# Kernel tuning notes

Measured on AMD Instinct MI355X. Metric: run time of the kernel, lower is better.

Reference implementation:

```python
import jax, jax.numpy as jnp
import numpy as np

N_CONS = 100_000
N_VAR = 200_000
N_EDGE = 2_000_000
EMB = 64
CONS_F = 5
VAR_F = 19
EDGE_F = 1
N_LAYERS = 2


def setup_inputs() -> dict:
    key = jax.random.key(0)
    ks = iter(jax.random.split(key, 48))
    def nrm(shape, scale=0.05):
        return jax.random.normal(next(ks), shape, dtype=jnp.float32) * scale
    inp = {}
    inp["cons_x"] = jax.random.normal(next(ks), (N_CONS, CONS_F), dtype=jnp.float32)
    inp["var_x"] = jax.random.normal(next(ks), (N_VAR, VAR_F), dtype=jnp.float32)
    row = jax.random.randint(next(ks), (N_EDGE,), 0, N_CONS, dtype=jnp.int32)
    col = jax.random.randint(next(ks), (N_EDGE,), 0, N_VAR, dtype=jnp.int32)
    inp["edge_index"] = jnp.stack([row, col], axis=0)
    inp["edge_attr"] = jax.random.normal(next(ks), (N_EDGE, EDGE_F), dtype=jnp.float32)
    inp["break_indicator"] = jax.random.uniform(next(ks), (N_VAR, 1), dtype=jnp.float32)
    # PreNormLayer affine params: y = (x + shift) * scale
    inp["cons_pn_shift"] = nrm((CONS_F,))
    inp["cons_pn_scale"] = 1.0 + nrm((CONS_F,))
    inp["var_pn_shift"] = nrm((VAR_F,))
    inp["var_pn_scale"] = 1.0 + nrm((VAR_F,))
    inp["edge_pn_shift"] = nrm((EDGE_F,))
    inp["edge_pn_scale"] = 1.0 + nrm((EDGE_F,))
    # embedding MLPs
    inp["cons_W1"] = nrm((CONS_F, EMB), 0.4)
    inp["cons_b1"] = nrm((EMB,))
    inp["cons_W2"] = nrm((EMB, EMB), 0.12)
    inp["cons_b2"] = nrm((EMB,))
    inp["var_W1"] = nrm((VAR_F, EMB), 0.22)
    inp["var_b1"] = nrm((EMB,))
    inp["var_W2"] = nrm((EMB, EMB), 0.12)
    inp["var_b2"] = nrm((EMB,))
    inp["break_W"] = nrm((1, EMB), 0.5)
    # SAGEConv params per layer: lin_l (neighbor mean, with bias), lin_r (root, no bias)
    inp["Wl_cv"] = nrm((N_LAYERS, EMB, EMB), 0.12)
    inp["bl_cv"] = nrm((N_LAYERS, EMB))
    inp["Wr_cv"] = nrm((N_LAYERS, EMB, EMB), 0.12)
    inp["Wl_vc"] = nrm((N_LAYERS, EMB, EMB), 0.12)
    inp["bl_vc"] = nrm((N_LAYERS, EMB))
    inp["Wr_vc"] = nrm((N_LAYERS, EMB, EMB), 0.12)
    return inp


def _embed(x, shift, scale, W1, b1, W2, b2):
    h = (x + shift) * scale
    h = jax.nn.relu(h @ W1 + b1)
    return jax.nn.relu(h @ W2 + b2)


def _sage(x_src, x_dst, src, dst, n_dst, Wl, bl, Wr):
    # gather source features per edge, mean-aggregate by destination (PyG SAGEConv mean aggr)
    msg = x_src[src]                                              # [E, emb]
    s = jax.ops.segment_sum(msg, dst, num_segments=n_dst)         # [n_dst, emb]
    cnt = jax.ops.segment_sum(jnp.ones((src.shape[0], 1), x_src.dtype), dst, num_segments=n_dst)
    mean = s / jnp.maximum(cnt, 1.0)
    return mean @ Wl + bl + x_dst @ Wr


def reference(cons_x, var_x, edge_index, edge_attr, break_indicator,
              cons_pn_shift, cons_pn_scale, var_pn_shift, var_pn_scale,
              edge_pn_shift, edge_pn_scale,
              cons_W1, cons_b1, cons_W2, cons_b2,
              var_W1, var_b1, var_W2, var_b2,
              break_W, Wl_cv, bl_cv, Wr_cv, Wl_vc, bl_vc, Wr_vc):
    row, col = edge_index[0], edge_index[1]
    cons = _embed(cons_x, cons_pn_shift, cons_pn_scale, cons_W1, cons_b1, cons_W2, cons_b2)
    var = _embed(var_x, var_pn_shift, var_pn_scale, var_W1, var_b1, var_W2, var_b2)
    _edge = (edge_attr + edge_pn_shift) * edge_pn_scale  # computed as in module; unused by SAGE convs
    var = var + break_indicator @ break_W
    n_cons, n_var = cons.shape[0], var.shape[0]
    for l in range(Wl_cv.shape[0]):
        # HeteroConv: both directions computed from the same x_dict, then ReLU
        new_var = jax.nn.relu(_sage(cons, var, row, col, n_var, Wl_cv[l], bl_cv[l], Wr_cv[l]))
        new_cons = jax.nn.relu(_sage(var, cons, col, row, n_cons, Wl_vc[l], bl_vc[l], Wr_vc[l]))
        cons, var = new_cons, new_var
    return var
```

## Files before the change

kernel.cpp:

```cpp
#include <hip/hip_runtime.h>

#define N_CONS 100000
#define N_VAR  200000
#define N_TOT  (N_CONS + N_VAR)
#define N_EDGE 2000000
#define EMB 64

#define VSH 10
#define NBV 196
#define CAPV 12288
#define CSH 9
#define NBC 196
#define CAPC 12288
#define CAPAV (CAPV + 3 * 1024)
#define CAPAC (CAPC + 3 * 512)
#define NB_VAR ((N_VAR + 63) / 64)
#define NB_CONS ((N_CONS + 63) / 64)

typedef unsigned short u16;
typedef __attribute__((ext_vector_type(8))) short bf16x8;
typedef __attribute__((ext_vector_type(4))) float f32x4;


__device__ __forceinline__ float b2f_lo(unsigned u) {
  union { unsigned i; float f; } c;
  c.i = u << 16;
  return c.f;
}
__device__ __forceinline__ float b2f_hi(unsigned u) {
  union { unsigned i; float f; } c;
  c.i = u & 0xFFFF0000u;
  return c.f;
}
__device__ __forceinline__ unsigned pack_bf2(float a, float b) {
  unsigned ua = __float_as_uint(a), ub = __float_as_uint(b);
  unsigned ra = (ua + 0x7FFFu + ((ua >> 16) & 1u)) >> 16;
  unsigned rb = (ub + 0x7FFFu + ((ub >> 16) & 1u)) >> 16;
  return ra | (rb << 16);
}
__device__ __forceinline__ u16 f2bf(float a) {
  unsigned ua = __float_as_uint(a);
  return (u16)((ua + 0x7FFFu + ((ua >> 16) & 1u)) >> 16);
}


__global__ __launch_bounds__(256) void csr_init(int* __restrict__ gcurV,
                                                int* __restrict__ gcurC,
                                                uint2* __restrict__ consEbf,
                                                uint2* __restrict__ varEbf,
                                                uint2* __restrict__ cons1bf) {
  int t = threadIdx.x;
  if (t < NBV) gcurV[t] = t * CAPV;
  if (t < NBC) gcurC[t] = t * CAPC;
  if (t < 16) consEbf[(size_t)N_CONS * 16 + t] = make_uint2(0u, 0u);
  else if (t < 32) varEbf[(size_t)N_VAR * 16 + (t - 16)] = make_uint2(0u, 0u);
  else if (t < 48) cons1bf[(size_t)N_CONS * 16 + (t - 32)] = make_uint2(0u, 0u);
}

__global__ __launch_bounds__(256) void bucket_scatter(
    const int* __restrict__ row, const int* __restrict__ col,
    int* __restrict__ gcurV, int* __restrict__ gcurC,
    int* __restrict__ pairV, int* __restrict__ pairC) {
  __shared__ int hV[NBV];
  __shared__ int hC[NBC];
  int tid = threadIdx.x;
  int chunk = (N_EDGE + gridDim.x - 1) / gridDim.x;
  int lo = blockIdx.x * chunk;
  int hi = min(N_EDGE, lo + chunk);
  for (int i = tid; i < NBV; i += 256) hV[i] = 0;
  for (int i = tid; i < NBC; i += 256) hC[i] = 0;
  __syncthreads();
  for (int e = lo + tid; e < hi; e += 256) {
    atomicAdd(&hV[col[e] >> VSH], 1);
    atomicAdd(&hC[row[e] >> CSH], 1);
  }
  __syncthreads();
  for (int i = tid; i < NBV; i += 256) {
    int c = hV[i];
    hV[i] = c ? atomicAdd(&gcurV[i], c) : 0;
  }
  for (int i = tid; i < NBC; i += 256) {
    int c = hC[i];
    hC[i] = c ? atomicAdd(&gcurC[i], c) : 0;
  }
  __syncthreads();
  for (int e = lo + tid; e < hi; e += 256) {
    int r = row[e], c = col[e];
    int p = atomicAdd(&hV[c >> VSH], 1);
    pairV[p] = (r << VSH) | (c & ((1 << VSH) - 1));
    int q = atomicAdd(&hC[r >> CSH], 1);
    pairC[q] = (c << CSH) | (r & ((1 << CSH) - 1));
  }
}

__global__ __launch_bounds__(1024) void local_csr(
    const int* __restrict__ pairV, const int* __restrict__ pairC,
    const int* __restrict__ gcurV, const int* __restrict__ gcurC,
    int* __restrict__ off, int* __restrict__ deg, int* __restrict__ adj) {
  __shared__ int cnt[1024];
  __shared__ int s[1024];
  __shared__ int cur[1024];
  int tid = threadIdx.x;
  int b = blockIdx.x;
  const int* pairs;
  int m, obase, nn, sh, zrow;
  int* offp;
  int* degp;
  if (b < NBV) {
    pairs = pairV + (size_t)b * CAPV;
    m = gcurV[b] - b * CAPV;
    obase = b * CAPAV;
    nn = min(1024, N_VAR - (b << 10));
    sh = VSH;
    zrow = N_CONS;
    offp = off + (b << 10);
    degp = deg + (b << 10);
  } else {
    int bb = b - NBV;
    pairs = pairC + (size_t)bb * CAPC;
    m = gcurC[bb] - bb * CAPC;
    obase = NBV * CAPAV + bb * CAPAC;
    nn = min(512, N_CONS - (bb << 9));
    sh = CSH;
    zrow = N_VAR;
    offp = off + N_VAR + (bb << 9);
    degp = deg + N_VAR + (bb << 9);
  }
  int mask = (1 << sh) - 1;
  cnt[tid] = 0;
  __syncthreads();
  for (int k = tid; k < m; k += 1024) atomicAdd(&cnt[pairs[k] & mask], 1);
  __syncthreads();
  int c = cnt[tid];
  int pc = (c + 3) & ~3;
  s[tid] = pc;
  __syncthreads();
  for (int d1 = 1; d1 < 1024; d1 <<= 1) {
    int x = (tid >= d1) ? s[tid - d1] : 0;
    __syncthreads();
    s[tid] += x;
    __syncthreads();
  }
  int start = obase + s[tid] - pc;
  cur[tid] = start;
  if (tid < nn) {
    offp[tid] = start;
    degp[tid] = c;
  }
  __syncthreads();
  for (int k = tid; k < m; k += 1024) {
    int pr = pairs[k];
    int p = atomicAdd(&cur[pr & mask], 1);
    adj[p] = pr >> sh;
  }
  for (int q = c; q < pc; ++q) adj[start + q] = zrow;
}


template <int F>
__global__ __launch_bounds__(256) void embed_mm(
    const float* __restrict__ x, const float* __restrict__ shift,
    const float* __restrict__ scale, const float* __restrict__ W1,
    const float* __restrict__ b1, const float* __restrict__ W2,
    const float* __restrict__ b2, const float* __restrict__ bi,
    const float* __restrict__ bW, u16* __restrict__ outbf, int n) {
  __shared__ float Xs[F * 68];
  __shared__ float W1s[F * 68];
  __shared__ u16 Hs[64][72];
  __shared__ u16 W2s[64][72];
  __shared__ float b1s[64], b2s[64], bWs[64], bis[64];
  int t = threadIdx.x;
  int v0 = blockIdx.x * 64;

  int sn = t & 63;
  int kq = t >> 6;
  {
    unsigned pk[8];
#pragma unroll
    for (int i = 0; i < 8; ++i) {
      float w0 = W2[(size_t)(kq * 16 + 2 * i) * 64 + sn];
      float w1 = W2[(size_t)(kq * 16 + 2 * i + 1) * 64 + sn];
      pk[i] = pack_bf2(w0, w1);
    }
    *(uint4*)&W2s[sn][kq * 16] = make_uint4(pk[0], pk[1], pk[2], pk[3]);
    *(uint4*)&W2s[sn][kq * 16 + 8] = make_uint4(pk[4], pk[5], pk[6], pk[7]);
  }
  for (int i = t; i < F * 64; i += 256) {
    int k = i >> 6, j = i & 63;
    W1s[k * 68 + j] = W1[i] * scale[k];
  }
  if (t < 64) {
    float acc = b1[t];
#pragma unroll
    for (int k = 0; k < F; ++k) acc += shift[k] * scale[k] * W1[k * 64 + t];
    b1s[t] = acc;
    b2s[t] = b2[t];
    bWs[t] = bW ? bW[t] : 0.f;
    bis[t] = (bi && v0 + t < n) ? bi[v0 + t] : 0.f;
  }
  for (int i = t; i < 64 * F; i += 256) {
    int row = i / F, k = i - row * F;
    int v = v0 + row;
    Xs[k * 68 + row] = (v < n) ? x[(size_t)v * F + k] : 0.f;
  }
  __syncthreads();

  int jt = t & 15;
  int vt = t >> 4;
  float c[4][4] = {};
#pragma unroll
  for (int k = 0; k < F; ++k) {
    float4 xv = *(const float4*)&Xs[k * 68 + vt * 4];
    float4 wv = *(const float4*)&W1s[k * 68 + jt * 4];
    c[0][0] += xv.x * wv.x; c[0][1] += xv.x * wv.y; c[0][2] += xv.x * wv.z; c[0][3] += xv.x * wv.w;
    c[1][0] += xv.y * wv.x; c[1][1] += xv.y * wv.y; c[1][2] += xv.y * wv.z; c[1][3] += xv.y * wv.w;
    c[2][0] += xv.z * wv.x; c[2][1] += xv.z * wv.y; c[2][2] += xv.z * wv.z; c[2][3] += xv.z * wv.w;
    c[3][0] += xv.w * wv.x; c[3][1] += xv.w * wv.y; c[3][2] += xv.w * wv.z; c[3][3] += xv.w * wv.w;
  }
#pragma unroll
  for (int i = 0; i < 4; ++i) {
    float h0 = fmaxf(c[i][0] + b1s[jt * 4 + 0], 0.f);
    float h1 = fmaxf(c[i][1] + b1s[jt * 4 + 1], 0.f);
    float h2 = fmaxf(c[i][2] + b1s[jt * 4 + 2], 0.f);
    float h3 = fmaxf(c[i][3] + b1s[jt * 4 + 3], 0.f);
    *(uint2*)&Hs[vt * 4 + i][jt * 4] = make_uint2(pack_bf2(h0, h1), pack_bf2(h2, h3));
  }
  __syncthreads();

  int l = t & 63;
  int w = t >> 6;
  int m0 = w * 16;
  int rA = m0 + (l & 15);
  int koffA = (l >> 4) * 8;
  f32x4 acc[4] = {};
  {
    bf16x8 a0 = *(const bf16x8*)&Hs[rA][koffA];
    bf16x8 a1 = *(const bf16x8*)&Hs[rA][32 + koffA];
#pragma unroll
    for (int cb = 0; cb < 4; ++cb) {
      int nB = cb * 16 + (l & 15);
      bf16x8 b0 = *(const bf16x8*)&W2s[nB][koffA];
      bf16x8 bb1 = *(const bf16x8*)&W2s[nB][32 + koffA];
      acc[cb] = __builtin_amdgcn_mfma_f32_16x16x32_bf16(a0, b0, acc[cb], 0, 0, 0);
      acc[cb] = __builtin_amdgcn_mfma_f32_16x16x32_bf16(a1, bb1, acc[cb], 0, 0, 0);
    }
  }
#pragma unroll
  for (int cb = 0; cb < 4; ++cb) {
    int colc = cb * 16 + (l & 15);
    float bias = b2s[colc];
    float bwv = bWs[colc];
#pragma unroll
    for (int j = 0; j < 4; ++j) {
      int rowc = m0 + (l >> 4) * 4 + j;
      int v = v0 + rowc;
      if (v < n) {
        float val = fmaxf(acc[cb][j] + bias, 0.f) + bis[rowc] * bwv;
        outbf[(size_t)v * 64 + colc] = f2bf(val);
      }
    }
  }
}


template <int OUTBF>
__device__ __forceinline__ void sage_body(
    const uint2* __restrict__ srcbf, const uint2* __restrict__ dstbf,
    const int* __restrict__ off, const int* __restrict__ deg,
    const int* __restrict__ adj, const float* __restrict__ Wl,
    const float* __restrict__ bl, const float* __restrict__ Wr,
    float* __restrict__ outf, u16* __restrict__ outbf, int n, int v0,
    u16 (*Hs)[72], u16 (*Ws)[72], float* bls) {
  int t = threadIdx.x;
  if (t < 64) bls[t] = bl[t];

  int sn = t & 63;
  int kq = t >> 6;
  {
    unsigned pk[8];
#pragma unroll
    for (int i = 0; i < 8; ++i) {
      float w0 = Wl[(size_t)(kq * 16 + 2 * i) * 64 + sn];
      float w1 = Wl[(size_t)(kq * 16 + 2 * i + 1) * 64 + sn];
      pk[i] = pack_bf2(w0, w1);
    }
    *(uint4*)&Ws[sn][kq * 16] = make_uint4(pk[0], pk[1], pk[2], pk[3]);
    *(uint4*)&Ws[sn][kq * 16 + 8] = make_uint4(pk[4], pk[5], pk[6], pk[7]);
  }

  int lane = t & 15;
  int g = t >> 4;
#pragma unroll
  for (int grp = 0; grp < 4; ++grp) {
    int r = grp * 16 + g;
    int v = v0 + r;
    float ax = 0.f, ay = 0.f, az = 0.f, aw = 0.f;
    if (v < n) {
      int s0 = off[v];
      int d = deg[v];
      int e4 = s0 + ((d + 3) & ~3);
      for (int i = s0; i < e4; i += 4) {
        int u0 = adj[i], u1 = adj[i + 1], u2 = adj[i + 2], u3 = adj[i + 3];
        uint2 a0 = srcbf[(size_t)u0 * 16 + lane];
        uint2 a1 = srcbf[(size_t)u1 * 16 + lane];
        uint2 a2 = srcbf[(size_t)u2 * 16 + lane];
        uint2 a3 = srcbf[(size_t)u3 * 16 + lane];
        ax += (b2f_lo(a0.x) + b2f_lo(a1.x)) + (b2f_lo(a2.x) + b2f_lo(a3.x));
        ay += (b2f_hi(a0.x) + b2f_hi(a1.x)) + (b2f_hi(a2.x) + b2f_hi(a3.x));
        az += (b2f_lo(a0.y) + b2f_lo(a1.y)) + (b2f_lo(a2.y) + b2f_lo(a3.y));
        aw += (b2f_hi(a0.y) + b2f_hi(a1.y)) + (b2f_hi(a2.y) + b2f_hi(a3.y));
      }
      float inv = (d > 0) ? 1.f / (float)d : 0.f;
      ax *= inv;
      ay *= inv;
      az *= inv;
      aw *= inv;
    }
    *(uint2*)&Hs[r][lane * 4] = make_uint2(pack_bf2(ax, ay), pack_bf2(az, aw));
  }
  __syncthreads();

  int l = t & 63;
  int w = t >> 6;
  int m0 = w * 16;
  int rA = m0 + (l & 15);
  int koffA = (l >> 4) * 8;
  f32x4 acc[4] = {};
  {
    bf16x8 a0 = *(const bf16x8*)&Hs[rA][koffA];
    bf16x8 a1 = *(const bf16x8*)&Hs[rA][32 + koffA];
#pragma unroll
    for (int cb = 0; cb < 4; ++cb) {
      int nB = cb * 16 + (l & 15);
      bf16x8 b0 = *(const bf16x8*)&Ws[nB][koffA];
      bf16x8 b1 = *(const bf16x8*)&Ws[nB][32 + koffA];
      acc[cb] = __builtin_amdgcn_mfma_f32_16x16x32_bf16(a0, b0, acc[cb], 0, 0, 0);
      acc[cb] = __builtin_amdgcn_mfma_f32_16x16x32_bf16(a1, b1, acc[cb], 0, 0, 0);
    }
  }
  __syncthreads();

#pragma unroll
  for (int r4 = 0; r4 < 4; ++r4) {
    int idx = t + 256 * r4;
    int rowi = idx >> 4, f4 = idx & 15;
    int v = v0 + rowi;
    uint2 val = (v < n) ? dstbf[(size_t)v * 16 + f4] : make_uint2(0u, 0u);
    *(uint2*)&Hs[rowi][f4 * 4] = val;
  }
  {
    unsigned pk[8];
#pragma unroll
    for (int i = 0; i < 8; ++i) {
      float w0 = Wr[(size_t)(kq * 16 + 2 * i) * 64 + sn];
      float w1 = Wr[(size_t)(kq * 16 + 2 * i + 1) * 64 + sn];
      pk[i] = pack_bf2(w0, w1);
    }
    *(uint4*)&Ws[sn][kq * 16] = make_uint4(pk[0], pk[1], pk[2], pk[3]);
    *(uint4*)&Ws[sn][kq * 16 + 8] = make_uint4(pk[4], pk[5], pk[6], pk[7]);
  }
  __syncthreads();

  {
    bf16x8 a0 = *(const bf16x8*)&Hs[rA][koffA];
    bf16x8 a1 = *(const bf16x8*)&Hs[rA][32 + koffA];
#pragma unroll
    for (int cb = 0; cb < 4; ++cb) {
      int nB = cb * 16 + (l & 15);
      bf16x8 b0 = *(const bf16x8*)&Ws[nB][koffA];
      bf16x8 b1 = *(const bf16x8*)&Ws[nB][32 + koffA];
      acc[cb] = __builtin_amdgcn_mfma_f32_16x16x32_bf16(a0, b0, acc[cb], 0, 0, 0);
      acc[cb] = __builtin_amdgcn_mfma_f32_16x16x32_bf16(a1, b1, acc[cb], 0, 0, 0);
    }
  }

#pragma unroll
  for (int cb = 0; cb < 4; ++cb) {
    int colc = cb * 16 + (l & 15);
    float bias = bls[colc];
#pragma unroll
    for (int j = 0; j < 4; ++j) {
      int rowc = m0 + (l >> 4) * 4 + j;
      int v = v0 + rowc;
      if (v < n) {
        float val = fmaxf(acc[cb][j] + bias, 0.f);
        if (OUTBF) {
          outbf[(size_t)v * 64 + colc] = f2bf(val);
        } else {
          outf[(size_t)v * 64 + colc] = val;
        }
      }
    }
  }
}

__global__ __launch_bounds__(256) void sage_l0(
    const uint2* __restrict__ consEbf, const uint2* __restrict__ varEbf,
    const int* __restrict__ off, const int* __restrict__ deg,
    const int* __restrict__ adj, const float* __restrict__ Wl_cv,
    const float* __restrict__ bl_cv, const float* __restrict__ Wr_cv,
    const float* __restrict__ Wl_vc, const float* __restrict__ bl_vc,
    const float* __restrict__ Wr_vc, u16* __restrict__ var1bf,
    u16* __restrict__ cons1bf) {
  __shared__ u16 Hs[64][72];
  __shared__ u16 Ws[64][72];
  __shared__ float bls[64];
  int b = blockIdx.x;
  if (b < NB_VAR) {
    sage_body<1>(consEbf, varEbf, off, deg, adj, Wl_cv, bl_cv, Wr_cv, nullptr,
                 var1bf, N_VAR, b * 64, Hs, Ws, bls);
  } else {
    sage_body<1>(varEbf, consEbf, off + N_VAR, deg + N_VAR, adj, Wl_vc, bl_vc,
                 Wr_vc, nullptr, cons1bf, N_CONS, (b - NB_VAR) * 64, Hs, Ws, bls);
  }
}

__global__ __launch_bounds__(256) void sage_l1(
    const uint2* __restrict__ cons1bf, const uint2* __restrict__ var1bf,
    const int* __restrict__ off, const int* __restrict__ deg,
    const int* __restrict__ adj, const float* __restrict__ Wl,
    const float* __restrict__ bl, const float* __restrict__ Wr,
    float* __restrict__ out) {
  __shared__ u16 Hs[64][72];
  __shared__ u16 Ws[64][72];
  __shared__ float bls[64];
  sage_body<0>(cons1bf, var1bf, off, deg, adj, Wl, bl, Wr, out, nullptr, N_VAR,
               blockIdx.x * 64, Hs, Ws, bls);
}


extern "C" void kernel_launch(void* const* d_in, const int* in_sizes, int n_in,
                              void* d_out, int out_size, void* d_ws, size_t ws_size,
                              hipStream_t stream) {
  const float* cons_x = (const float*)d_in[0];
  const float* var_x  = (const float*)d_in[1];
  const int*   eidx   = (const int*)d_in[2];
  const float* bi     = (const float*)d_in[4];
  const float* c_sh   = (const float*)d_in[5];
  const float* c_sc   = (const float*)d_in[6];
  const float* v_sh   = (const float*)d_in[7];
  const float* v_sc   = (const float*)d_in[8];
  const float* cW1 = (const float*)d_in[11];
  const float* cb1 = (const float*)d_in[12];
  const float* cW2 = (const float*)d_in[13];
  const float* cb2 = (const float*)d_in[14];
  const float* vW1 = (const float*)d_in[15];
  const float* vb1 = (const float*)d_in[16];
  const float* vW2 = (const float*)d_in[17];
  const float* vb2 = (const float*)d_in[18];
  const float* bW  = (const float*)d_in[19];
  const float* Wl_cv = (const float*)d_in[20];
  const float* bl_cv = (const float*)d_in[21];
  const float* Wr_cv = (const float*)d_in[22];
  const float* Wl_vc = (const float*)d_in[23];
  const float* bl_vc = (const float*)d_in[24];
  const float* Wr_vc = (const float*)d_in[25];

  const int* row = eidx;
  const int* col = eidx + N_EDGE;

  char* ws = (char*)d_ws;
  size_t o = 0;
  auto alloc = [&](size_t bytes) {
    char* p = ws + o;
    o = (o + bytes + 255) & ~(size_t)255;
    return p;
  };
  int* off   = (int*)alloc((size_t)N_TOT * sizeof(int));
  int* deg   = (int*)alloc((size_t)N_TOT * sizeof(int));
  int* adj   = (int*)alloc(((size_t)NBV * CAPAV + (size_t)NBC * CAPAC) * sizeof(int));
  int* pairV = (int*)alloc((size_t)NBV * CAPV * sizeof(int));
  int* pairC = (int*)alloc((size_t)NBC * CAPC * sizeof(int));
  int* gcurV = (int*)alloc(256 * sizeof(int));
  int* gcurC = (int*)alloc(256 * sizeof(int));
  uint2* consEbf = (uint2*)alloc((size_t)(N_CONS + 1) * EMB * 2);
  uint2* varEbf  = (uint2*)alloc((size_t)(N_VAR + 1) * EMB * 2);
  uint2* cons1bf = (uint2*)alloc((size_t)(N_CONS + 1) * EMB * 2);
  uint2* var1bf  = (uint2*)alloc((size_t)N_VAR * EMB * 2);
  float* var_out = (float*)d_out;

  csr_init<<<1, 256, 0, stream>>>(gcurV, gcurC, consEbf, varEbf, cons1bf);
  bucket_scatter<<<512, 256, 0, stream>>>(row, col, gcurV, gcurC, pairV, pairC);
  local_csr<<<NBV + NBC, 1024, 0, stream>>>(pairV, pairC, gcurV, gcurC, off,
                                            deg, adj);

  embed_mm<5><<<NB_CONS, 256, 0, stream>>>(cons_x, c_sh, c_sc, cW1, cb1, cW2,
                                           cb2, nullptr, nullptr, (u16*)consEbf,
                                           N_CONS);
  embed_mm<19><<<NB_VAR, 256, 0, stream>>>(var_x, v_sh, v_sc, vW1, vb1, vW2,
                                           vb2, bi, bW, (u16*)varEbf, N_VAR);

  sage_l0<<<NB_VAR + NB_CONS, 256, 0, stream>>>(
      consEbf, varEbf, off, deg, adj, Wl_cv, bl_cv, Wr_cv, Wl_vc, bl_vc, Wr_vc,
      (u16*)var1bf, (u16*)cons1bf);
  sage_l1<<<NB_VAR, 256, 0, stream>>>(cons1bf, var1bf, off, deg, adj,
                                      Wl_cv + 4096, bl_cv + 64, Wr_cv + 4096,
                                      var_out);
}
```

Measured before the change: 258.9 us.

## Fuse edge scatter and embedding MLPs into one front kernel; dynamic row queue in SAGE

Replaces the csr_init, bucket_scatter and two embed_mm launches with one fused_front kernel that assigns blocks by index to scatter, cons-embed, var-embed or pad-row zeroing. The bucket cursors become zero-based counters cleared with a memset, so the per-bucket base offset is added in the scatter. In the SAGE body, 16-lane groups now pull destination rows from a shared atomic work counter instead of a fixed four-row assignment, to balance degree skew within a block. This removes launch gaps and lets the scatter overlap the embedding work, at the cost of a larger shared-memory footprint per block and extra LDS atomics.

```diff
diff --git a/kernel.cpp b/kernel.cpp
--- a/kernel.cpp
+++ b/kernel.cpp
@@ -16,6 +16,7 @@
 #define CAPAC (CAPC + 3 * 512)
 #define NB_VAR ((N_VAR + 63) / 64)
 #define NB_CONS ((N_CONS + 63) / 64)
+#define NB_SCAT 512
 
 typedef unsigned short u16;
 typedef __attribute__((ext_vector_type(8))) short bf16x8;
@@ -44,28 +45,15 @@
 }
 
 
-__global__ __launch_bounds__(256) void csr_init(int* __restrict__ gcurV,
-                                                int* __restrict__ gcurC,
-                                                uint2* __restrict__ consEbf,
-                                                uint2* __restrict__ varEbf,
-                                                uint2* __restrict__ cons1bf) {
-  int t = threadIdx.x;
-  if (t < NBV) gcurV[t] = t * CAPV;
-  if (t < NBC) gcurC[t] = t * CAPC;
-  if (t < 16) consEbf[(size_t)N_CONS * 16 + t] = make_uint2(0u, 0u);
-  else if (t < 32) varEbf[(size_t)N_VAR * 16 + (t - 16)] = make_uint2(0u, 0u);
-  else if (t < 48) cons1bf[(size_t)N_CONS * 16 + (t - 32)] = make_uint2(0u, 0u);
-}
-
-__global__ __launch_bounds__(256) void bucket_scatter(
-    const int* __restrict__ row, const int* __restrict__ col,
-    int* __restrict__ gcurV, int* __restrict__ gcurC,
-    int* __restrict__ pairV, int* __restrict__ pairC) {
-  __shared__ int hV[NBV];
-  __shared__ int hC[NBC];
+__device__ __forceinline__ void scatter_body(
+    int b, char* smem, const int* __restrict__ row, const int* __restrict__ col,
+    int* __restrict__ gcurV, int* __restrict__ gcurC, int* __restrict__ pairV,
+    int* __restrict__ pairC) {
+  int* hV = (int*)smem;
+  int* hC = hV + NBV;
   int tid = threadIdx.x;
-  int chunk = (N_EDGE + gridDim.x - 1) / gridDim.x;
-  int lo = blockIdx.x * chunk;
+  int chunk = (N_EDGE + NB_SCAT - 1) / NB_SCAT;
+  int lo = b * chunk;
   int hi = min(N_EDGE, lo + chunk);
   for (int i = tid; i < NBV; i += 256) hV[i] = 0;
   for (int i = tid; i < NBC; i += 256) hC[i] = 0;
@@ -77,11 +65,11 @@
   __syncthreads();
   for (int i = tid; i < NBV; i += 256) {
     int c = hV[i];
-    hV[i] = c ? atomicAdd(&gcurV[i], c) : 0;
+    hV[i] = c ? (i * CAPV + atomicAdd(&gcurV[i], c)) : 0;
   }
   for (int i = tid; i < NBC; i += 256) {
     int c = hC[i];
-    hC[i] = c ? atomicAdd(&gcurC[i], c) : 0;
+    hC[i] = c ? (i * CAPC + atomicAdd(&gcurC[i], c)) : 0;
   }
   __syncthreads();
   for (int e = lo + tid; e < hi; e += 256) {
@@ -92,6 +80,150 @@
     pairC[q] = (c << CSH) | (r & ((1 << CSH) - 1));
   }
 }
+
+template <int F>
+__device__ __forceinline__ void embed_body(
+    int blk, char* smem, const float* __restrict__ x,
+    const float* __restrict__ shift, const float* __restrict__ scale,
+    const float* __restrict__ W1, const float* __restrict__ b1,
+    const float* __restrict__ W2, const float* __restrict__ b2,
+    const float* __restrict__ bi, const float* __restrict__ bW,
+    u16* __restrict__ outbf, int n) {
+  float* Xs = (float*)smem;
+  float* W1s = Xs + F * 68;
+  u16 (*Hs)[72] = (u16(*)[72])(W1s + F * 68);
+  u16 (*W2s)[72] = (u16(*)[72])((char*)Hs + 64 * 72 * 2);
+  float* b1s = (float*)((char*)W2s + 64 * 72 * 2);
+  float* b2s = b1s + 64;
+  float* bWs = b2s + 64;
+  float* bis = bWs + 64;
+  int t = threadIdx.x;
+  int v0 = blk * 64;
+
+  int sn = t & 63;
+  int kq = t >> 6;
+  {
+    unsigned pk[8];
+#pragma unroll
+    for (int i = 0; i < 8; ++i) {
+      float w0 = W2[(size_t)(kq * 16 + 2 * i) * 64 + sn];
+      float w1 = W2[(size_t)(kq * 16 + 2 * i + 1) * 64 + sn];
+      pk[i] = pack_bf2(w0, w1);
+    }
+    *(uint4*)&W2s[sn][kq * 16] = make_uint4(pk[0], pk[1], pk[2], pk[3]);
+    *(uint4*)&W2s[sn][kq * 16 + 8] = make_uint4(pk[4], pk[5], pk[6], pk[7]);
+  }
+  for (int i = t; i < F * 64; i += 256) {
+    int k = i >> 6, j = i & 63;
+    W1s[k * 68 + j] = W1[i] * scale[k];
+  }
+  if (t < 64) {
+    float acc = b1[t];
+#pragma unroll
+    for (int k = 0; k < F; ++k) acc += shift[k] * scale[k] * W1[k * 64 + t];
+    b1s[t] = acc;
+    b2s[t] = b2[t];
+    bWs[t] = bW ? bW[t] : 0.f;
+    bis[t] = (bi && v0 + t < n) ? bi[v0 + t] : 0.f;
+  }
+  for (int i = t; i < 64 * F; i += 256) {
+    int r = i / F, k = i - r * F;
+    int v = v0 + r;
+    Xs[k * 68 + r] = (v < n) ? x[(size_t)v * F + k] : 0.f;
+  }
+  __syncthreads();
+
+  int jt = t & 15;
+  int vt = t >> 4;
+  float c[4][4] = {};
+#pragma unroll
+  for (int k = 0; k < F; ++k) {
+    float4 xv = *(const float4*)&Xs[k * 68 + vt * 4];
+    float4 wv = *(const float4*)&W1s[k * 68 + jt * 4];
+    c[0][0] += xv.x * wv.x; c[0][1] += xv.x * wv.y; c[0][2] += xv.x * wv.z; c[0][3] += xv.x * wv.w;
+    c[1][0] += xv.y * wv.x; c[1][1] += xv.y * wv.y; c[1][2] += xv.y * wv.z; c[1][3] += xv.y * wv.w;
+    c[2][0] += xv.z * wv.x; c[2][1] += xv.z * wv.y; c[2][2] += xv.z * wv.z; c[2][3] += xv.z * wv.w;
+    c[3][0] += xv.w * wv.x; c[3][1] += xv.w * wv.y; c[3][2] += xv.w * wv.z; c[3][3] += xv.w * wv.w;
+  }
+#pragma unroll
+  for (int i = 0; i < 4; ++i) {
+    float h0 = fmaxf(c[i][0] + b1s[jt * 4 + 0], 0.f);
+    float h1 = fmaxf(c[i][1] + b1s[jt * 4 + 1], 0.f);
+    float h2 = fmaxf(c[i][2] + b1s[jt * 4 + 2], 0.f);
+    float h3 = fmaxf(c[i][3] + b1s[jt * 4 + 3], 0.f);
+    *(uint2*)&Hs[vt * 4 + i][jt * 4] = make_uint2(pack_bf2(h0, h1), pack_bf2(h2, h3));
+  }
+  __syncthreads();
+
+  int l = t & 63;
+  int w = t >> 6;
+  int m0 = w * 16;
+  int rA = m0 + (l & 15);
+  int koffA = (l >> 4) * 8;
+  f32x4 acc[4] = {};
+  {
+    bf16x8 a0 = *(const bf16x8*)&Hs[rA][koffA];
+    bf16x8 a1 = *(const bf16x8*)&Hs[rA][32 + koffA];
+#pragma unroll
+    for (int cb = 0; cb < 4; ++cb) {
+      int nB = cb * 16 + (l & 15);
+      bf16x8 b0 = *(const bf16x8*)&W2s[nB][koffA];
+      bf16x8 bb1 = *(const bf16x8*)&W2s[nB][32 + koffA];
+      acc[cb] = __builtin_amdgcn_mfma_f32_16x16x32_bf16(a0, b0, acc[cb], 0, 0, 0);
+      acc[cb] = __builtin_amdgcn_mfma_f32_16x16x32_bf16(a1, bb1, acc[cb], 0, 0, 0);
+    }
+  }
+#pragma unroll
+  for (int cb = 0; cb < 4; ++cb) {
+    int colc = cb * 16 + (l & 15);
+    float bias = b2s[colc];
+    float bwv = bWs[colc];
+#pragma unroll
+    for (int j = 0; j < 4; ++j) {
+      int rowc = m0 + (l >> 4) * 4 + j;
+      int v = v0 + rowc;
+      if (v < n) {
+        float val = fmaxf(acc[cb][j] + bias, 0.f) + bis[rowc] * bwv;
+        outbf[(size_t)v * 64 + colc] = f2bf(val);
+      }
+    }
+  }
+}
+
+#define FRONT_SMEM 29824
+
+__global__ __launch_bounds__(256) void fused_front(
+    const int* __restrict__ row, const int* __restrict__ col,
+    int* __restrict__ gcurV, int* __restrict__ gcurC, int* __restrict__ pairV,
+    int* __restrict__ pairC, const float* __restrict__ cons_x,
+    const float* __restrict__ c_sh, const float* __restrict__ c_sc,
+    const float* __restrict__ cW1, const float* __restrict__ cb1,
+    const float* __restrict__ cW2, const float* __restrict__ cb2,
+    const float* __restrict__ var_x, const float* __restrict__ v_sh,
+    const float* __restrict__ v_sc, const float* __restrict__ vW1,
+    const float* __restrict__ vb1, const float* __restrict__ vW2,
+    const float* __restrict__ vb2, const float* __restrict__ bi,
+    const float* __restrict__ bW, u16* __restrict__ consEbf,
+    u16* __restrict__ varEbf, uint2* __restrict__ padrows0,
+    uint2* __restrict__ padrows1, uint2* __restrict__ padrows2) {
+  __shared__ __align__(16) char smem[FRONT_SMEM];
+  int b = blockIdx.x;
+  if (b < NB_SCAT) {
+    scatter_body(b, smem, row, col, gcurV, gcurC, pairV, pairC);
+  } else if (b < NB_SCAT + NB_CONS) {
+    embed_body<5>(b - NB_SCAT, smem, cons_x, c_sh, c_sc, cW1, cb1, cW2, cb2,
+                  nullptr, nullptr, consEbf, N_CONS);
+  } else if (b < NB_SCAT + NB_CONS + NB_VAR) {
+    embed_body<19>(b - NB_SCAT - NB_CONS, smem, var_x, v_sh, v_sc, vW1, vb1,
+                   vW2, vb2, bi, bW, varEbf, N_VAR);
+  } else {
+    int t = threadIdx.x;
+    if (t < 16) padrows0[t] = make_uint2(0u, 0u);
+    else if (t < 32) padrows1[t - 16] = make_uint2(0u, 0u);
+    else if (t < 48) padrows2[t - 32] = make_uint2(0u, 0u);
+  }
+}
+
 
 __global__ __launch_bounds__(1024) void local_csr(
     const int* __restrict__ pairV, const int* __restrict__ pairC,
@@ -108,7 +240,7 @@
   int* degp;
   if (b < NBV) {
     pairs = pairV + (size_t)b * CAPV;
-    m = gcurV[b] - b * CAPV;
+    m = gcurV[b];
     obase = b * CAPAV;
     nn = min(1024, N_VAR - (b << 10));
     sh = VSH;
@@ -118,7 +250,7 @@
   } else {
     int bb = b - NBV;
     pairs = pairC + (size_t)bb * CAPC;
-    m = gcurC[bb] - bb * CAPC;
+    m = gcurC[bb];
     obase = NBV * CAPAV + bb * CAPAC;
     nn = min(512, N_CONS - (bb << 9));
     sh = CSH;
@@ -154,112 +286,6 @@
     adj[p] = pr >> sh;
   }
   for (int q = c; q < pc; ++q) adj[start + q] = zrow;
-}
-
-
-template <int F>
-__global__ __launch_bounds__(256) void embed_mm(
-    const float* __restrict__ x, const float* __restrict__ shift,
-    const float* __restrict__ scale, const float* __restrict__ W1,
-    const float* __restrict__ b1, const float* __restrict__ W2,
-    const float* __restrict__ b2, const float* __restrict__ bi,
-    const float* __restrict__ bW, u16* __restrict__ outbf, int n) {
-  __shared__ float Xs[F * 68];
-  __shared__ float W1s[F * 68];
-  __shared__ u16 Hs[64][72];
-  __shared__ u16 W2s[64][72];
-  __shared__ float b1s[64], b2s[64], bWs[64], bis[64];
-  int t = threadIdx.x;
-  int v0 = blockIdx.x * 64;
-
-  int sn = t & 63;
-  int kq = t >> 6;
-  {
-    unsigned pk[8];
-#pragma unroll
-    for (int i = 0; i < 8; ++i) {
-      float w0 = W2[(size_t)(kq * 16 + 2 * i) * 64 + sn];
-      float w1 = W2[(size_t)(kq * 16 + 2 * i + 1) * 64 + sn];
-      pk[i] = pack_bf2(w0, w1);
-    }
-    *(uint4*)&W2s[sn][kq * 16] = make_uint4(pk[0], pk[1], pk[2], pk[3]);
-    *(uint4*)&W2s[sn][kq * 16 + 8] = make_uint4(pk[4], pk[5], pk[6], pk[7]);
-  }
-  for (int i = t; i < F * 64; i += 256) {
-    int k = i >> 6, j = i & 63;
-    W1s[k * 68 + j] = W1[i] * scale[k];
-  }
-  if (t < 64) {
-    float acc = b1[t];
-#pragma unroll
-    for (int k = 0; k < F; ++k) acc += shift[k] * scale[k] * W1[k * 64 + t];
-    b1s[t] = acc;
-    b2s[t] = b2[t];
-    bWs[t] = bW ? bW[t] : 0.f;
-    bis[t] = (bi && v0 + t < n) ? bi[v0 + t] : 0.f;
-  }
-  for (int i = t; i < 64 * F; i += 256) {
-    int row = i / F, k = i - row * F;
-    int v = v0 + row;
-    Xs[k * 68 + row] = (v < n) ? x[(size_t)v * F + k] : 0.f;
-  }
-  __syncthreads();
-
-  int jt = t & 15;
-  int vt = t >> 4;
-  float c[4][4] = {};
-#pragma unroll
-  for (int k = 0; k < F; ++k) {
-    float4 xv = *(const float4*)&Xs[k * 68 + vt * 4];
-    float4 wv = *(const float4*)&W1s[k * 68 + jt * 4];
-    c[0][0] += xv.x * wv.x; c[0][1] += xv.x * wv.y; c[0][2] += xv.x * wv.z; c[0][3] += xv.x * wv.w;
-    c[1][0] += xv.y * wv.x; c[1][1] += xv.y * wv.y; c[1][2] += xv.y * wv.z; c[1][3] += xv.y * wv.w;
-    c[2][0] += xv.z * wv.x; c[2][1] += xv.z * wv.y; c[2][2] += xv.z * wv.z; c[2][3] += xv.z * wv.w;
-    c[3][0] += xv.w * wv.x; c[3][1] += xv.w * wv.y; c[3][2] += xv.w * wv.z; c[3][3] += xv.w * wv.w;
-  }
-#pragma unroll
-  for (int i = 0; i < 4; ++i) {
-    float h0 = fmaxf(c[i][0] + b1s[jt * 4 + 0], 0.f);
-    float h1 = fmaxf(c[i][1] + b1s[jt * 4 + 1], 0.f);
-    float h2 = fmaxf(c[i][2] + b1s[jt * 4 + 2], 0.f);
-    float h3 = fmaxf(c[i][3] + b1s[jt * 4 + 3], 0.f);
-    *(uint2*)&Hs[vt * 4 + i][jt * 4] = make_uint2(pack_bf2(h0, h1), pack_bf2(h2, h3));
-  }
-  __syncthreads();
-
-  int l = t & 63;
-  int w = t >> 6;
-  int m0 = w * 16;
-  int rA = m0 + (l & 15);
-  int koffA = (l >> 4) * 8;
-  f32x4 acc[4] = {};
-  {
-    bf16x8 a0 = *(const bf16x8*)&Hs[rA][koffA];
-    bf16x8 a1 = *(const bf16x8*)&Hs[rA][32 + koffA];
-#pragma unroll
-    for (int cb = 0; cb < 4; ++cb) {
-      int nB = cb * 16 + (l & 15);
-      bf16x8 b0 = *(const bf16x8*)&W2s[nB][koffA];
-      bf16x8 bb1 = *(const bf16x8*)&W2s[nB][32 + koffA];
-      acc[cb] = __builtin_amdgcn_mfma_f32_16x16x32_bf16(a0, b0, acc[cb], 0, 0, 0);
-      acc[cb] = __builtin_amdgcn_mfma_f32_16x16x32_bf16(a1, bb1, acc[cb], 0, 0, 0);
-    }
-  }
-#pragma unroll
-  for (int cb = 0; cb < 4; ++cb) {
-    int colc = cb * 16 + (l & 15);
-    float bias = b2s[colc];
-    float bwv = bWs[colc];
-#pragma unroll
-    for (int j = 0; j < 4; ++j) {
-      int rowc = m0 + (l >> 4) * 4 + j;
-      int v = v0 + rowc;
-      if (v < n) {
-        float val = fmaxf(acc[cb][j] + bias, 0.f) + bis[rowc] * bwv;
-        outbf[(size_t)v * 64 + colc] = f2bf(val);
-      }
-    }
-  }
 }
 
 
@@ -270,9 +296,10 @@
     const int* __restrict__ adj, const float* __restrict__ Wl,
     const float* __restrict__ bl, const float* __restrict__ Wr,
     float* __restrict__ outf, u16* __restrict__ outbf, int n, int v0,
-    u16 (*Hs)[72], u16 (*Ws)[72], float* bls) {
+    u16 (*Hs)[72], u16 (*Ws)[72], float* bls, int* wq) {
   int t = threadIdx.x;
   if (t < 64) bls[t] = bl[t];
+  if (t == 0) *wq = 0;
 
   int sn = t & 63;
   int kq = t >> 6;
@@ -287,12 +314,14 @@
     *(uint4*)&Ws[sn][kq * 16] = make_uint4(pk[0], pk[1], pk[2], pk[3]);
     *(uint4*)&Ws[sn][kq * 16 + 8] = make_uint4(pk[4], pk[5], pk[6], pk[7]);
   }
+  __syncthreads();
 
   int lane = t & 15;
-  int g = t >> 4;
-#pragma unroll
-  for (int grp = 0; grp < 4; ++grp) {
-    int r = grp * 16 + g;
+  while (true) {
+    int r = 0;
+    if (lane == 0) r = atomicAdd(wq, 1);
+    r = __shfl(r, 0, 16);
+    if (r >= 64) break;
     int v = v0 + r;
     float ax = 0.f, ay = 0.f, az = 0.f, aw = 0.f;
     if (v < n) {
@@ -405,13 +434,15 @@
   __shared__ u16 Hs[64][72];
   __shared__ u16 Ws[64][72];
   __shared__ float bls[64];
+  __shared__ int wq;
   int b = blockIdx.x;
   if (b < NB_VAR) {
     sage_body<1>(consEbf, varEbf, off, deg, adj, Wl_cv, bl_cv, Wr_cv, nullptr,
-                 var1bf, N_VAR, b * 64, Hs, Ws, bls);
+                 var1bf, N_VAR, b * 64, Hs, Ws, bls, &wq);
   } else {
     sage_body<1>(varEbf, consEbf, off + N_VAR, deg + N_VAR, adj, Wl_vc, bl_vc,
-                 Wr_vc, nullptr, cons1bf, N_CONS, (b - NB_VAR) * 64, Hs, Ws, bls);
+                 Wr_vc, nullptr, cons1bf, N_CONS, (b - NB_VAR) * 64, Hs, Ws,
+                 bls, &wq);
   }
 }
 
@@ -424,8 +455,9 @@
   __shared__ u16 Hs[64][72];
   __shared__ u16 Ws[64][72];
   __shared__ float bls[64];
+  __shared__ int wq;
   sage_body<0>(cons1bf, var1bf, off, deg, adj, Wl, bl, Wr, out, nullptr, N_VAR,
-               blockIdx.x * 64, Hs, Ws, bls);
+               blockIdx.x * 64, Hs, Ws, bls, &wq);
 }
 
 
@@ -479,16 +511,16 @@
   uint2* var1bf  = (uint2*)alloc((size_t)N_VAR * EMB * 2);
   float* var_out = (float*)d_out;
 
-  csr_init<<<1, 256, 0, stream>>>(gcurV, gcurC, consEbf, varEbf, cons1bf);
-  bucket_scatter<<<512, 256, 0, stream>>>(row, col, gcurV, gcurC, pairV, pairC);
+  hipMemsetAsync(gcurV, 0, 2048, stream);
+
+  fused_front<<<NB_SCAT + NB_CONS + NB_VAR + 1, 256, 0, stream>>>(
+      row, col, gcurV, gcurC, pairV, pairC, cons_x, c_sh, c_sc, cW1, cb1, cW2,
+      cb2, var_x, v_sh, v_sc, vW1, vb1, vW2, vb2, bi, bW, (u16*)consEbf,
+      (u16*)varEbf, consEbf + (size_t)N_CONS * 16, varEbf + (size_t)N_VAR * 16,
+      cons1bf + (size_t)N_CONS * 16);
+
   local_csr<<<NBV + NBC, 1024, 0, stream>>>(pairV, pairC, gcurV, gcurC, off,
                                             deg, adj);
-
-  embed_mm<5><<<NB_CONS, 256, 0, stream>>>(cons_x, c_sh, c_sc, cW1, cb1, cW2,
-                                           cb2, nullptr, nullptr, (u16*)consEbf,
-                                           N_CONS);
-  embed_mm<19><<<NB_VAR, 256, 0, stream>>>(var_x, v_sh, v_sc, vW1, vb1, vW2,
-                                           vb2, bi, bW, (u16*)varEbf, N_VAR);
 
   sage_l0<<<NB_VAR + NB_CONS, 256, 0, stream>>>(
       consEbf, varEbf, off, deg, adj, Wl_cv, bl_cv, Wr_cv, Wl_vc, bl_vc, Wr_vc,
```

New measurement: 248.3 us. 4.1% less time.
